# Kernel optimization log

Measured on AMD Instinct MI355X. Metric: run time of the kernel, lower is better.

The kernel has to match this reference:

```python
import jax, jax.numpy as jnp
import numpy as np

EPS = 1e-6
GROUPS = 32
SCALE = 1.0 / np.float32(512.0) ** 0.5


def setup_inputs() -> dict:
    key = jax.random.key(0)
    ks = jax.random.split(key, 8)
    b, c, h, w = 4, 512, 64, 64
    std = 0.02
    return {
        "x": jax.random.normal(ks[0], (b, c, h, w), dtype=jnp.float32),
        "gamma": jnp.ones((c,), jnp.float32),
        "beta": jnp.zeros((c,), jnp.float32),
        "wq_w": jax.random.normal(ks[1], (c, c), jnp.float32) * std,
        "wq_b": jax.random.normal(ks[2], (c,), jnp.float32) * std,
        "wk_w": jax.random.normal(ks[3], (c, c), jnp.float32) * std,
        "wk_b": jax.random.normal(ks[4], (c,), jnp.float32) * std,
        "wv_w": jax.random.normal(ks[5], (c, c), jnp.float32) * std,
        "wv_b": jax.random.normal(ks[6], (c,), jnp.float32) * std,
        "out_w": jax.random.normal(ks[7], (c, c), jnp.float32) * std,
        "out_b": jnp.zeros((c,), jnp.float32),
    }


def reference(x, gamma, beta, wq_w, wq_b, wk_w, wk_b, wv_w, wv_b, out_w, out_b):
    b, c, h, w = x.shape
    # GroupNorm(32 groups, eps=1e-6, affine)
    xg = x.reshape(b, GROUPS, c // GROUPS, h, w)
    mean = xg.mean(axis=(2, 3, 4), keepdims=True)
    var = ((xg - mean) ** 2).mean(axis=(2, 3, 4), keepdims=True)
    xn = ((xg - mean) * jax.lax.rsqrt(var + EPS)).reshape(b, c, h, w)
    xn = xn * gamma[None, :, None, None] + beta[None, :, None, None]
    # flatten spatial -> tokens: [b, N, c]
    t = xn.reshape(b, c, h * w).transpose(0, 2, 1)
    q = t @ wq_w.T + wq_b
    k = t @ wk_w.T + wk_b
    v = t @ wv_w.T + wv_b
    scores = jnp.einsum('bnc,bmc->bnm', q, k) * SCALE  # [b, N, N]
    attn = jax.nn.softmax(scores, axis=2)
    o = jnp.einsum('bnm,bmc->bnc', attn, v)
    o = o @ out_w.T + out_b
    return o.transpose(0, 2, 1).reshape(b, c, h, w) + x
```

## Files before the change

kernel.cpp:

```cpp
#include <hip/hip_runtime.h>
#include <hip/hip_fp8.h>

typedef unsigned short u16;
typedef unsigned char u8;
typedef short bf16x8 __attribute__((ext_vector_type(8)));
typedef float f32x4 __attribute__((ext_vector_type(4)));
typedef u16 u16x4 __attribute__((ext_vector_type(4)));

#define SCALE_Q 0.044194173824159216f

#define BAR() asm volatile("s_waitcnt lgkmcnt(0)\n\ts_barrier" ::: "memory")

__device__ __forceinline__ u16 f2b(float f){
  unsigned u = __float_as_uint(f);
  u += 0x7fffu + ((u >> 16) & 1u);
  return (u16)(u >> 16);
}

__device__ __forceinline__ u8 f2e4(float f){
  return __hip_fp8_e4m3(f).__x;
}

__device__ __forceinline__ void gload16(const void* g, void* l){
  __builtin_amdgcn_global_load_lds(
      (const __attribute__((address_space(1))) void*)g,
      (__attribute__((address_space(3))) void*)l, 16, 0, 0);
}

__device__ __forceinline__ float qsum16(float v){
  v += __shfl_xor(v, 1); v += __shfl_xor(v, 2);
  v += __shfl_xor(v, 4); v += __shfl_xor(v, 8);
  return v;
}

__global__ __launch_bounds__(256) void gn_stats(const float* __restrict__ x,
                                                float* __restrict__ stats){
  int bg = blockIdx.x;
  const float4* p4 = (const float4*)(x + (size_t)bg * 65536);
  float s = 0.f, ss = 0.f;
  for (int i = threadIdx.x; i < 16384; i += 256){
    float4 v = p4[i];
    s  += v.x + v.y + v.z + v.w;
    ss += v.x*v.x + v.y*v.y + v.z*v.z + v.w*v.w;
  }
  for (int off = 32; off; off >>= 1){
    s  += __shfl_down(s, off);
    ss += __shfl_down(ss, off);
  }
  __shared__ float as_[4], bs_[4];
  int wid = threadIdx.x >> 6, lid = threadIdx.x & 63;
  if (lid == 0){ as_[wid] = s; bs_[wid] = ss; }
  __syncthreads();
  if (threadIdx.x == 0){
    float S = as_[0]+as_[1]+as_[2]+as_[3], SS = bs_[0]+bs_[1]+bs_[2]+bs_[3];
    float mean = S * (1.f/65536.f);
    float var  = SS * (1.f/65536.f) - mean*mean;
    stats[2*bg]   = mean;
    stats[2*bg+1] = rsqrtf(var + 1e-6f);
  }
}

__global__ __launch_bounds__(256) void gn_apply_T(const float* __restrict__ x,
                                                  const float* __restrict__ stats,
                                                  const float* __restrict__ gamma,
                                                  const float* __restrict__ beta,
                                                  u16* __restrict__ t){
  __shared__ float tile[32][33];
  int nb = blockIdx.x, cb = blockIdx.y, b = blockIdx.z;
  int tx = threadIdx.x & 31, ty = threadIdx.x >> 5;
  int n0 = nb * 32, c0 = cb * 32;
  #pragma unroll
  for (int i = 0; i < 4; i++){
    int ch = c0 + ty + i*8;
    float mean = stats[2*((b<<5) + (ch>>4))];
    float rstd = stats[2*((b<<5) + (ch>>4)) + 1];
    float v = x[(((size_t)b*512 + ch) << 12) + n0 + tx];
    tile[ty + i*8][tx] = (v - mean) * rstd * gamma[ch] + beta[ch];
  }
  __syncthreads();
  #pragma unroll
  for (int i = 0; i < 4; i++){
    int n = n0 + ty + i*8;
    int ch = c0 + tx;
    t[((size_t)((b<<12) + n))*512 + ch] = f2b(tile[tx][ty + i*8]);
  }
}

__global__ __launch_bounds__(256) void w2bf(const float* __restrict__ a,
                                            const float* __restrict__ b,
                                            const float* __restrict__ c,
                                            const float* __restrict__ d,
                                            u16* __restrict__ o){
  int idx = blockIdx.x * 256 + threadIdx.x;
  int which = idx >> 16;
  const float4* src = (const float4*)(which == 0 ? a : which == 1 ? b : which == 2 ? c : d);
  float4 v = src[idx & 65535];
  u16x4 pk;
  pk.x = f2b(v.x); pk.y = f2b(v.y); pk.z = f2b(v.z); pk.w = f2b(v.w);
  *(u16x4*)(o + (size_t)idx*4) = pk;
}

__global__ __launch_bounds__(256, 2) void qkv_gemm(const u16* __restrict__ A,
                                                   const u16* __restrict__ Wcat,
                                                   const float* __restrict__ qbias,
                                                   const float* __restrict__ kbias,
                                                   const float* __restrict__ vbias,
                                                   u8* __restrict__ qo,
                                                   u8* __restrict__ ko,
                                                   u16* __restrict__ vo){
  __shared__ __align__(16) u16 As[128*32];
  __shared__ __align__(16) u16 Bs[128*32];
  const int t = threadIdx.x;
  const int w = t >> 6, ln = t & 63;
  const int wr = w >> 1, wc = w & 1;
  const int q4 = ln >> 4, l15 = ln & 15;
  const int y = blockIdx.y;
  const int mat = y >> 2, yb = y & 3;
  const u16* Ab = A    + (size_t)blockIdx.x * 128 * 512;
  const u16* Bb = Wcat + (size_t)y * 128 * 512;
  f32x4 acc[4][4];
  #pragma unroll
  for (int i = 0; i < 4; i++)
    #pragma unroll
    for (int j = 0; j < 4; j++){
      acc[i][j][0]=0.f; acc[i][j][1]=0.f; acc[i][j][2]=0.f; acc[i][j][3]=0.f;
    }
  for (int kt = 0; kt < 16; ++kt){
    #pragma unroll
    for (int i = 0; i < 2; i++){
      int idx = i*256 + t;
      gload16(Ab + (size_t)(idx>>2)*512 + kt*32 + (idx&3)*8, As + (size_t)idx*8);
      gload16(Bb + (size_t)(idx>>2)*512 + kt*32 + (idx&3)*8, Bs + (size_t)idx*8);
    }
    __syncthreads();
    bf16x8 af[4], bf[4];
    #pragma unroll
    for (int mt = 0; mt < 4; mt++)
      af[mt] = *(const bf16x8*)(As + (wr*64 + mt*16 + l15)*32 + q4*8);
    #pragma unroll
    for (int nt = 0; nt < 4; nt++)
      bf[nt] = *(const bf16x8*)(Bs + (wc*64 + nt*16 + l15)*32 + q4*8);
    #pragma unroll
    for (int mt = 0; mt < 4; mt++)
      #pragma unroll
      for (int nt = 0; nt < 4; nt++)
        acc[mt][nt] = __builtin_amdgcn_mfma_f32_16x16x32_bf16(af[mt], bf[nt], acc[mt][nt], 0, 0, 0);
    __syncthreads();
  }
  const int row0 = blockIdx.x*128 + wr*64;
  const int col0 = yb*128 + wc*64;
  if (mat == 0){
    #pragma unroll
    for (int nt = 0; nt < 4; nt++){
      int n = col0 + nt*16 + l15;
      float bv = qbias[n];
      #pragma unroll
      for (int mt = 0; mt < 4; mt++){
        int m0 = row0 + mt*16 + q4*4;
        #pragma unroll
        for (int r = 0; r < 4; r++)
          qo[(size_t)(m0 + r)*512 + n] = f2e4(acc[mt][nt][r] + bv);
      }
    }
  } else if (mat == 1){
    #pragma unroll
    for (int nt = 0; nt < 4; nt++){
      int n = col0 + nt*16 + l15;
      float bv = kbias[n];
      int ks = n >> 5, ch = n & 31;
      #pragma unroll
      for (int mt = 0; mt < 4; mt++){
        int m0 = row0 + mt*16 + q4*4;
        #pragma unroll
        for (int r = 0; r < 4; r++){
          int m = m0 + r;
          int bb = m >> 12, tok = m & 4095;
          int kr = tok & 31, tile = tok >> 5;
          int chunk = (ch >> 3) ^ ((kr >> 2) & 3);
          size_t addr = ((((size_t)bb*128 + tile) << 14)) + ks*1024 + kr*32 + chunk*8 + (ch & 7);
          ko[addr] = f2e4(acc[mt][nt][r] + bv);
        }
      }
    }
  } else {
    #pragma unroll
    for (int nt = 0; nt < 4; nt++){
      int n = col0 + nt*16 + l15;
      float bv = vbias[n];
      #pragma unroll
      for (int mt = 0; mt < 4; mt++){
        int m0 = row0 + mt*16 + q4*4;
        int bb = m0 >> 12, tok = m0 & 4095;
        u16x4 pk;
        pk.x = f2b(acc[mt][nt][0] + bv);
        pk.y = f2b(acc[mt][nt][1] + bv);
        pk.z = f2b(acc[mt][nt][2] + bv);
        pk.w = f2b(acc[mt][nt][3] + bv);
        size_t base = (((size_t)bb*128 + (tok>>5))*512 + n)*32 + (tok&31);
        *(u16x4*)(vo + base) = pk;
      }
    }
  }
}

__global__ __launch_bounds__(256, 2) void out_gemm(const u16* __restrict__ A,
                                                   const u16* __restrict__ Bw,
                                                   const float* __restrict__ bias,
                                                   float* __restrict__ out,
                                                   const float* __restrict__ resid){
  __shared__ __align__(16) u16 As[128*32];
  __shared__ __align__(16) u16 Bs[128*32];
  const int t = threadIdx.x;
  const int w = t >> 6, ln = t & 63;
  const int wr = w >> 1, wc = w & 1;
  const int q4 = ln >> 4, l15 = ln & 15;
  const u16* Ab = A  + (size_t)blockIdx.x * 128 * 512;
  const u16* Bb = Bw + (size_t)blockIdx.y * 128 * 512;
  f32x4 acc[4][4];
  #pragma unroll
  for (int i = 0; i < 4; i++)
    #pragma unroll
    for (int j = 0; j < 4; j++){
      acc[i][j][0]=0.f; acc[i][j][1]=0.f; acc[i][j][2]=0.f; acc[i][j][3]=0.f;
    }
  for (int kt = 0; kt < 16; ++kt){
    #pragma unroll
    for (int i = 0; i < 2; i++){
      int idx = i*256 + t;
      gload16(Ab + (size_t)(idx>>2)*512 + kt*32 + (idx&3)*8, As + (size_t)idx*8);
      gload16(Bb + (size_t)(idx>>2)*512 + kt*32 + (idx&3)*8, Bs + (size_t)idx*8);
    }
    __syncthreads();
    bf16x8 af[4], bf[4];
    #pragma unroll
    for (int mt = 0; mt < 4; mt++)
      af[mt] = *(const bf16x8*)(As + (wr*64 + mt*16 + l15)*32 + q4*8);
    #pragma unroll
    for (int nt = 0; nt < 4; nt++)
      bf[nt] = *(const bf16x8*)(Bs + (wc*64 + nt*16 + l15)*32 + q4*8);
    #pragma unroll
    for (int mt = 0; mt < 4; mt++)
      #pragma unroll
      for (int nt = 0; nt < 4; nt++)
        acc[mt][nt] = __builtin_amdgcn_mfma_f32_16x16x32_bf16(af[mt], bf[nt], acc[mt][nt], 0, 0, 0);
    __syncthreads();
  }
  const int row0 = blockIdx.x*128 + wr*64;
  const int col0 = blockIdx.y*128 + wc*64;
  #pragma unroll
  for (int nt = 0; nt < 4; nt++){
    int n = col0 + nt*16 + l15;
    float bv = bias[n];
    #pragma unroll
    for (int mt = 0; mt < 4; mt++){
      int m0 = row0 + mt*16 + q4*4;
      int bb = m0 >> 12, tok = m0 & 4095;
      size_t base = (((size_t)(bb*512 + n)) << 12) + tok;
      float4 xr = *(const float4*)(resid + base);
      float4 ov;
      ov.x = acc[mt][nt][0] + bv + xr.x;
      ov.y = acc[mt][nt][1] + bv + xr.y;
      ov.z = acc[mt][nt][2] + bv + xr.z;
      ov.w = acc[mt][nt][3] + bv + xr.w;
      *(float4*)(out + base) = ov;
    }
  }
}

__global__ __launch_bounds__(256, 2) void attn_fwd(const u8* __restrict__ q,
                                                   const u8* __restrict__ kt,
                                                   const u16* __restrict__ vt,
                                                   u16* __restrict__ outO){
  __shared__ __align__(16) u8 Kb[2][16384];
  __shared__ __align__(16) u16 Pb[32*40];
  __shared__ __align__(16) float lL[64];

  const int t = threadIdx.x, w = t >> 6, ln = t & 63;
  const int q4 = ln >> 4, l15 = ln & 15;
  const int rt = w >> 1, chh = w & 1;
  const int b = blockIdx.y, q0 = blockIdx.x * 32;
  const u8*  kbase = kt + ((size_t)b << 21);
  const u16* vbase = vt + ((size_t)b << 21);

  long qf[16];
  {
    const u8* qr = q + (size_t)((b<<12) + q0 + rt*16 + l15) * 512;
    #pragma unroll
    for (int ks = 0; ks < 16; ks++) qf[ks] = *(const long*)(qr + ks*32 + q4*8);
  }
  f32x4 oacc[2][8];
  #pragma unroll
  for (int i = 0; i < 2; i++)
    #pragma unroll
    for (int j = 0; j < 8; j++){
      oacc[i][j][0]=0.f; oacc[i][j][1]=0.f; oacc[i][j][2]=0.f; oacc[i][j][3]=0.f;
    }
  f32x4 lrow; lrow[0]=0.f; lrow[1]=0.f; lrow[2]=0.f; lrow[3]=0.f;

  const int krow = chh*16 + l15;
  const int kcho = (q4 ^ ((krow >> 2) & 3)) << 3;

  #pragma unroll
  for (int i = 0; i < 4; i++){
    int ci = i*256 + t;
    gload16(kbase + (size_t)ci*16, &Kb[0][ci*16]);
  }
  __syncthreads();

  #pragma unroll 1
  for (int j = 0; j < 128; ++j){
    {
      const u8* kn = kbase + ((size_t)((j + 1) & 127) << 14);
      u8* kd = Kb[(j + 1) & 1];
      #pragma unroll
      for (int i = 0; i < 4; i++){
        int ci = i*256 + t;
        gload16(kn + (size_t)ci*16, kd + ci*16);
      }
    }
    bf16x8 vf[8];
    {
      const u16* vtile = vbase + ((size_t)j << 14);
      #pragma unroll
      for (int ct = 0; ct < 8; ct++)
        vf[ct] = *(const bf16x8*)(vtile + (128*w + ct*16 + l15)*32 + q4*8);
    }
    const u8* Kp = Kb[j & 1];
    f32x4 s; s[0]=0.f; s[1]=0.f; s[2]=0.f; s[3]=0.f;
    #pragma unroll
    for (int ks = 0; ks < 16; ks++){
      long kf = *(const long*)(Kp + ks*1024 + krow*32 + kcho);
      s = __builtin_amdgcn_mfma_f32_16x16x32_fp8_fp8(qf[ks], kf, s, 0, 0, 0);
    }
    #pragma unroll
    for (int r = 0; r < 4; r++){
      float e = __expf(s[r] * SCALE_Q);
      lrow[r] += e;
      Pb[(rt*16 + q4*4 + r)*40 + chh*16 + l15] = f2b(e);
    }
    BAR();
    {
      bf16x8 pf0 = *(const bf16x8*)(Pb + l15*40 + q4*8);
      bf16x8 pf1 = *(const bf16x8*)(Pb + (16 + l15)*40 + q4*8);
      #pragma unroll
      for (int ct = 0; ct < 8; ct++){
        oacc[0][ct] = __builtin_amdgcn_mfma_f32_16x16x32_bf16(pf0, vf[ct], oacc[0][ct], 0, 0, 0);
        oacc[1][ct] = __builtin_amdgcn_mfma_f32_16x16x32_bf16(pf1, vf[ct], oacc[1][ct], 0, 0, 0);
      }
    }
    __syncthreads();
  }

  {
    f32x4 ls;
    #pragma unroll
    for (int r = 0; r < 4; r++) ls[r] = qsum16(lrow[r]);
    if (l15 == 0) *(f32x4*)&lL[chh*32 + rt*16 + q4*4] = ls;
  }
  __syncthreads();
  #pragma unroll
  for (int rr = 0; rr < 2; rr++){
    #pragma unroll
    for (int r = 0; r < 4; r++){
      int row = rr*16 + q4*4 + r;
      float inv = 1.f / (lL[row] + lL[32 + row]);
      u16* op = outO + ((size_t)b << 21) + (size_t)(q0 + row)*512 + 128*w + l15;
      #pragma unroll
      for (int ct = 0; ct < 8; ct++)
        op[ct*16] = f2b(oacc[rr][ct][r] * inv);
    }
  }
}

extern "C" void kernel_launch(void* const* d_in, const int* in_sizes, int n_in,
                              void* d_out, int out_size, void* d_ws, size_t ws_size,
                              hipStream_t stream){
  const float* x     = (const float*)d_in[0];
  const float* gamma = (const float*)d_in[1];
  const float* beta  = (const float*)d_in[2];
  const float* wq_w  = (const float*)d_in[3];
  const float* wq_b  = (const float*)d_in[4];
  const float* wk_w  = (const float*)d_in[5];
  const float* wk_b  = (const float*)d_in[6];
  const float* wv_w  = (const float*)d_in[7];
  const float* wv_b  = (const float*)d_in[8];
  const float* out_w = (const float*)d_in[9];
  const float* out_b = (const float*)d_in[10];

  char* ws = (char*)d_ws;
  float* stats = (float*)ws;
  u16* tbuf = (u16*)(ws + 4096);
  size_t off = 4096 + (size_t)16*1024*1024;
  u16* Wcat = (u16*)(ws + off); off += (size_t)4*512*512*2;
  u8*  qb   = (u8*)(ws + off);  off += (size_t)16*1024*1024;
  u8*  ktb  = (u8*)(ws + off);  off += (size_t)16*1024*1024;
  u16* vtb  = (u16*)(ws + off); off += (size_t)16*1024*1024;

  gn_stats<<<128, 256, 0, stream>>>(x, stats);
  gn_apply_T<<<dim3(128, 16, 4), 256, 0, stream>>>(x, stats, gamma, beta, tbuf);
  w2bf<<<1024, 256, 0, stream>>>(wq_w, wk_w, wv_w, out_w, Wcat);
  u16* Wo = Wcat + 3*512*512;
  qkv_gemm<<<dim3(128, 12), 256, 0, stream>>>(tbuf, Wcat, wq_b, wk_b, wv_b,
                                              qb, ktb, vtb);
  attn_fwd<<<dim3(128, 4), 256, 0, stream>>>(qb, ktb, vtb, tbuf);
  out_gemm<<<dim3(128, 4), 256, 0, stream>>>(tbuf, Wo, out_b, (float*)d_out, x);
}
```

Before: 364.5 us.

## Use FP8 for V and P in attention with 64-key tiles and LDS-staged K/V stores

The V matrix and the softmax probabilities P move from bf16 to fp8 e4m3, so the PV product also runs on fp8 MFMA with K=32 per instruction. The key tile per iteration doubles to 64, which halves the loop count and barrier overhead, and the QK accumulation is split across independent accumulators. The QKV GEMM epilogue now stages K and V through shared memory and writes them out as coalesced 16-byte stores in the new swizzled layouts, replacing the old scattered byte stores. The cost is lower precision in P and V and twice as much LDS for the K double buffer.

```diff
diff --git a/kernel.cpp b/kernel.cpp
--- a/kernel.cpp
+++ b/kernel.cpp
@@ -3,6 +3,7 @@
 
 typedef unsigned short u16;
 typedef unsigned char u8;
+typedef unsigned int u32;
 typedef short bf16x8 __attribute__((ext_vector_type(8)));
 typedef float f32x4 __attribute__((ext_vector_type(4)));
 typedef u16 u16x4 __attribute__((ext_vector_type(4)));
@@ -107,16 +108,18 @@
                                                    const float* __restrict__ vbias,
                                                    u8* __restrict__ qo,
                                                    u8* __restrict__ ko,
-                                                   u16* __restrict__ vo){
-  __shared__ __align__(16) u16 As[128*32];
-  __shared__ __align__(16) u16 Bs[128*32];
+                                                   u8* __restrict__ vo){
+  __shared__ __align__(16) u16 SMEM[8192];
+  u16* As = SMEM;
+  u16* Bs = SMEM + 4096;
   const int t = threadIdx.x;
   const int w = t >> 6, ln = t & 63;
   const int wr = w >> 1, wc = w & 1;
   const int q4 = ln >> 4, l15 = ln & 15;
   const int y = blockIdx.y;
   const int mat = y >> 2, yb = y & 3;
-  const u16* Ab = A    + (size_t)blockIdx.x * 128 * 512;
+  const int row0 = blockIdx.x * 128;
+  const u16* Ab = A    + (size_t)row0 * 512;
   const u16* Bb = Wcat + (size_t)y * 128 * 512;
   f32x4 acc[4][4];
   #pragma unroll
@@ -147,8 +150,11 @@
         acc[mt][nt] = __builtin_amdgcn_mfma_f32_16x16x32_bf16(af[mt], bf[nt], acc[mt][nt], 0, 0, 0);
     __syncthreads();
   }
-  const int row0 = blockIdx.x*128 + wr*64;
+  const int bb = row0 >> 12;
+  const int tile0 = (row0 >> 6) & 63;
   const int col0 = yb*128 + wc*64;
+  u8* Ls = (u8*)SMEM;
+
   if (mat == 0){
     #pragma unroll
     for (int nt = 0; nt < 4; nt++){
@@ -156,7 +162,7 @@
       float bv = qbias[n];
       #pragma unroll
       for (int mt = 0; mt < 4; mt++){
-        int m0 = row0 + mt*16 + q4*4;
+        int m0 = row0 + wr*64 + mt*16 + q4*4;
         #pragma unroll
         for (int r = 0; r < 4; r++)
           qo[(size_t)(m0 + r)*512 + n] = f2e4(acc[mt][nt][r] + bv);
@@ -167,38 +173,52 @@
     for (int nt = 0; nt < 4; nt++){
       int n = col0 + nt*16 + l15;
       float bv = kbias[n];
-      int ks = n >> 5, ch = n & 31;
+      int ksl = wc*2 + (nt >> 1);
+      int c3  = ((nt & 1)*2 + (l15 >> 3));
       #pragma unroll
       for (int mt = 0; mt < 4; mt++){
-        int m0 = row0 + mt*16 + q4*4;
         #pragma unroll
         for (int r = 0; r < 4; r++){
-          int m = m0 + r;
-          int bb = m >> 12, tok = m & 4095;
-          int kr = tok & 31, tile = tok >> 5;
-          int chunk = (ch >> 3) ^ ((kr >> 2) & 3);
-          size_t addr = ((((size_t)bb*128 + tile) << 14)) + ks*1024 + kr*32 + chunk*8 + (ch & 7);
-          ko[addr] = f2e4(acc[mt][nt][r] + bv);
+          int kr = mt*16 + q4*4 + r;
+          int chunk = c3 ^ ((kr >> 2) & 3);
+          Ls[(wr*4 + ksl)*2048 + kr*32 + chunk*8 + (l15 & 7)] = f2e4(acc[mt][nt][r] + bv);
         }
       }
+    }
+    __syncthreads();
+    #pragma unroll
+    for (int i = 0; i < 4; i++){
+      int ci = i*256 + t;
+      int ri = ci >> 7, t2 = ri >> 2, ksl2 = ri & 3;
+      u8* dst = ko + ((size_t)(bb*64 + tile0 + t2))*32768
+                   + (size_t)(yb*4 + ksl2)*2048 + (size_t)(ci & 127)*16;
+      *(float4*)dst = *(const float4*)(Ls + (size_t)ci*16);
     }
   } else {
     #pragma unroll
     for (int nt = 0; nt < 4; nt++){
       int n = col0 + nt*16 + l15;
       float bv = vbias[n];
+      int nl = n & 127;
       #pragma unroll
       for (int mt = 0; mt < 4; mt++){
-        int m0 = row0 + mt*16 + q4*4;
-        int bb = m0 >> 12, tok = m0 & 4095;
-        u16x4 pk;
-        pk.x = f2b(acc[mt][nt][0] + bv);
-        pk.y = f2b(acc[mt][nt][1] + bv);
-        pk.z = f2b(acc[mt][nt][2] + bv);
-        pk.w = f2b(acc[mt][nt][3] + bv);
-        size_t base = (((size_t)bb*128 + (tok>>5))*512 + n)*32 + (tok&31);
-        *(u16x4*)(vo + base) = pk;
-      }
+        int kv = mt*16 + q4*4;
+        u32 pk = (u32)f2e4(acc[mt][nt][0] + bv)
+               | ((u32)f2e4(acc[mt][nt][1] + bv) << 8)
+               | ((u32)f2e4(acc[mt][nt][2] + bv) << 16)
+               | ((u32)f2e4(acc[mt][nt][3] + bv) << 24);
+        int phys = (kv >> 3) ^ (n & 7);
+        *(u32*)(Ls + wr*8192 + nl*64 + phys*8 + (kv & 4)) = pk;
+      }
+    }
+    __syncthreads();
+    #pragma unroll
+    for (int i = 0; i < 4; i++){
+      int ci = i*256 + t;
+      int t2 = ci >> 9;
+      u8* dst = vo + ((size_t)(bb*64 + tile0 + t2))*32768
+                   + (size_t)yb*8192 + (size_t)(ci & 511)*16;
+      *(float4*)dst = *(const float4*)(Ls + (size_t)ci*16);
     }
   }
 }
@@ -269,18 +289,18 @@
 
 __global__ __launch_bounds__(256, 2) void attn_fwd(const u8* __restrict__ q,
                                                    const u8* __restrict__ kt,
-                                                   const u16* __restrict__ vt,
+                                                   const u8* __restrict__ vt,
                                                    u16* __restrict__ outO){
-  __shared__ __align__(16) u8 Kb[2][16384];
-  __shared__ __align__(16) u16 Pb[32*40];
+  __shared__ __align__(16) u8 Kb[2][32768];
+  __shared__ __align__(16) u8 Pb[32*72];
   __shared__ __align__(16) float lL[64];
 
   const int t = threadIdx.x, w = t >> 6, ln = t & 63;
   const int q4 = ln >> 4, l15 = ln & 15;
   const int rt = w >> 1, chh = w & 1;
   const int b = blockIdx.y, q0 = blockIdx.x * 32;
-  const u8*  kbase = kt + ((size_t)b << 21);
-  const u16* vbase = vt + ((size_t)b << 21);
+  const u8* kbase = kt + ((size_t)b << 21);
+  const u8* vbase = vt + ((size_t)b << 21);
 
   long qf[16];
   {
@@ -297,55 +317,82 @@
     }
   f32x4 lrow; lrow[0]=0.f; lrow[1]=0.f; lrow[2]=0.f; lrow[3]=0.f;
 
-  const int krow = chh*16 + l15;
-  const int kcho = (q4 ^ ((krow >> 2) & 3)) << 3;
-
-  #pragma unroll
-  for (int i = 0; i < 4; i++){
+  const int kr0 = chh*32 + l15,  kr1 = chh*32 + 16 + l15;
+  const int ko0 = kr0*32 + ((q4 ^ ((kr0 >> 2) & 3)) << 3);
+  const int ko1 = kr1*32 + ((q4 ^ ((kr1 >> 2) & 3)) << 3);
+
+  #pragma unroll
+  for (int i = 0; i < 8; i++){
     int ci = i*256 + t;
     gload16(kbase + (size_t)ci*16, &Kb[0][ci*16]);
   }
   __syncthreads();
 
   #pragma unroll 1
-  for (int j = 0; j < 128; ++j){
+  for (int j = 0; j < 64; ++j){
     {
-      const u8* kn = kbase + ((size_t)((j + 1) & 127) << 14);
+      const u8* kn = kbase + ((size_t)((j + 1) & 63) << 15);
       u8* kd = Kb[(j + 1) & 1];
       #pragma unroll
-      for (int i = 0; i < 4; i++){
+      for (int i = 0; i < 8; i++){
         int ci = i*256 + t;
         gload16(kn + (size_t)ci*16, kd + ci*16);
       }
     }
-    bf16x8 vf[8];
+    long vf0[8], vf1[8];
     {
-      const u16* vtile = vbase + ((size_t)j << 14);
-      #pragma unroll
-      for (int ct = 0; ct < 8; ct++)
-        vf[ct] = *(const bf16x8*)(vtile + (128*w + ct*16 + l15)*32 + q4*8);
+      const u8* vtile = vbase + ((size_t)j << 15);
+      #pragma unroll
+      for (int ct = 0; ct < 8; ct++){
+        int ch = 128*w + ct*16 + l15;
+        int swz = ch & 7;
+        const u8* vr = vtile + (size_t)ch*64;
+        vf0[ct] = *(const long*)(vr + ((q4 ^ swz) << 3));
+        vf1[ct] = *(const long*)(vr + (((4 + q4) ^ swz) << 3));
+      }
     }
     const u8* Kp = Kb[j & 1];
-    f32x4 s; s[0]=0.f; s[1]=0.f; s[2]=0.f; s[3]=0.f;
-    #pragma unroll
-    for (int ks = 0; ks < 16; ks++){
-      long kf = *(const long*)(Kp + ks*1024 + krow*32 + kcho);
-      s = __builtin_amdgcn_mfma_f32_16x16x32_fp8_fp8(qf[ks], kf, s, 0, 0, 0);
+    f32x4 sA0, sA1, sB0, sB1;
+    sA0[0]=0.f;sA0[1]=0.f;sA0[2]=0.f;sA0[3]=0.f;
+    sA1[0]=0.f;sA1[1]=0.f;sA1[2]=0.f;sA1[3]=0.f;
+    sB0[0]=0.f;sB0[1]=0.f;sB0[2]=0.f;sB0[3]=0.f;
+    sB1[0]=0.f;sB1[1]=0.f;sB1[2]=0.f;sB1[3]=0.f;
+    #pragma unroll
+    for (int k2 = 0; k2 < 8; k2++){
+      const u8* e0 = Kp + (2*k2)*2048;
+      const u8* e1 = Kp + (2*k2 + 1)*2048;
+      long ka0 = *(const long*)(e0 + ko0);
+      long kb0 = *(const long*)(e0 + ko1);
+      long ka1 = *(const long*)(e1 + ko0);
+      long kb1 = *(const long*)(e1 + ko1);
+      sA0 = __builtin_amdgcn_mfma_f32_16x16x32_fp8_fp8(qf[2*k2],   ka0, sA0, 0, 0, 0);
+      sB0 = __builtin_amdgcn_mfma_f32_16x16x32_fp8_fp8(qf[2*k2],   kb0, sB0, 0, 0, 0);
+      sA1 = __builtin_amdgcn_mfma_f32_16x16x32_fp8_fp8(qf[2*k2+1], ka1, sA1, 0, 0, 0);
+      sB1 = __builtin_amdgcn_mfma_f32_16x16x32_fp8_fp8(qf[2*k2+1], kb1, sB1, 0, 0, 0);
     }
     #pragma unroll
     for (int r = 0; r < 4; r++){
-      float e = __expf(s[r] * SCALE_Q);
-      lrow[r] += e;
-      Pb[(rt*16 + q4*4 + r)*40 + chh*16 + l15] = f2b(e);
+      float e0 = __expf((sA0[r] + sA1[r]) * SCALE_Q);
+      float e1 = __expf((sB0[r] + sB1[r]) * SCALE_Q);
+      lrow[r] += e0 + e1;
+      int row = rt*16 + q4*4 + r;
+      Pb[row*72 + chh*32 + l15]      = f2e4(e0);
+      Pb[row*72 + chh*32 + 16 + l15] = f2e4(e1);
     }
     BAR();
     {
-      bf16x8 pf0 = *(const bf16x8*)(Pb + l15*40 + q4*8);
-      bf16x8 pf1 = *(const bf16x8*)(Pb + (16 + l15)*40 + q4*8);
+      long pf00 = *(const long*)(Pb + l15*72 + q4*8);
+      long pf01 = *(const long*)(Pb + l15*72 + 32 + q4*8);
+      long pf10 = *(const long*)(Pb + (16 + l15)*72 + q4*8);
+      long pf11 = *(const long*)(Pb + (16 + l15)*72 + 32 + q4*8);
       #pragma unroll
       for (int ct = 0; ct < 8; ct++){
-        oacc[0][ct] = __builtin_amdgcn_mfma_f32_16x16x32_bf16(pf0, vf[ct], oacc[0][ct], 0, 0, 0);
-        oacc[1][ct] = __builtin_amdgcn_mfma_f32_16x16x32_bf16(pf1, vf[ct], oacc[1][ct], 0, 0, 0);
+        f32x4 a0 = oacc[0][ct], a1 = oacc[1][ct];
+        a0 = __builtin_amdgcn_mfma_f32_16x16x32_fp8_fp8(pf00, vf0[ct], a0, 0, 0, 0);
+        a1 = __builtin_amdgcn_mfma_f32_16x16x32_fp8_fp8(pf10, vf0[ct], a1, 0, 0, 0);
+        a0 = __builtin_amdgcn_mfma_f32_16x16x32_fp8_fp8(pf01, vf1[ct], a0, 0, 0, 0);
+        a1 = __builtin_amdgcn_mfma_f32_16x16x32_fp8_fp8(pf11, vf1[ct], a1, 0, 0, 0);
+        oacc[0][ct] = a0; oacc[1][ct] = a1;
       }
     }
     __syncthreads();
@@ -394,7 +441,7 @@
   u16* Wcat = (u16*)(ws + off); off += (size_t)4*512*512*2;
   u8*  qb   = (u8*)(ws + off);  off += (size_t)16*1024*1024;
   u8*  ktb  = (u8*)(ws + off);  off += (size_t)16*1024*1024;
-  u16* vtb  = (u16*)(ws + off); off += (size_t)16*1024*1024;
+  u8*  vtb  = (u8*)(ws + off);  off += (size_t)16*1024*1024;
 
   gn_stats<<<128, 256, 0, stream>>>(x, stats);
   gn_apply_T<<<dim3(128, 16, 4), 256, 0, stream>>>(x, stats, gamma, beta, tbuf);
```

Result: faster. 325.3 us (-10.8%).
